# Kernel tuning notes

Hardware: AMD Instinct MI355X
Metric: run time of the kernel (lower is better)

The kernel has to match this reference:

```python
import jax, jax.numpy as jnp
import numpy as np

D_MODEL = 1024
N_HEAD = 16
ATT_DIM = D_MODEL // N_HEAD


def setup_inputs() -> dict:
    key = jax.random.key(0)
    ks = jax.random.split(key, 7)
    B, S = 2, 2048
    q = jax.random.normal(ks[0], (B, S, D_MODEL), dtype=jnp.float32)
    k = jax.random.normal(ks[1], (B, S, D_MODEL), dtype=jnp.float32)
    v = jax.random.normal(ks[2], (B, S, D_MODEL), dtype=jnp.float32)
    # per-head projection weights, stored as [H, d_model, att_dim] (x @ W form)
    scale_qkv = float(np.sqrt(6.0 / (D_MODEL + ATT_DIM)))  # xavier_uniform
    Wq = jax.random.uniform(ks[3], (N_HEAD, D_MODEL, ATT_DIM), jnp.float32, -scale_qkv, scale_qkv)
    Wk = jax.random.uniform(ks[4], (N_HEAD, D_MODEL, ATT_DIM), jnp.float32, -scale_qkv, scale_qkv)
    Wv = jax.random.uniform(ks[5], (N_HEAD, D_MODEL, ATT_DIM), jnp.float32, -scale_qkv, scale_qkv)
    scale_o = float(np.sqrt(6.0 / (D_MODEL + D_MODEL)))
    Wo = jax.random.uniform(ks[6], (D_MODEL, D_MODEL), jnp.float32, -scale_o, scale_o)
    return {"q": q, "k": k, "v": v, "Wq": Wq, "Wk": Wk, "Wv": Wv, "Wo": Wo}


def reference(q, k, v, Wq, Wk, Wv, Wo):
    # per-head projections, batched over heads: [H,B,S,E]
    qh = jnp.einsum('bsd,hde->hbse', q, Wq)
    kh = jnp.einsum('bsd,hde->hbse', k, Wk)
    vh = jnp.einsum('bsd,hde->hbse', v, Wv)
    # NOTE: original divides by att_dim (not sqrt(att_dim))
    scores = jnp.einsum('hbqe,hbke->hbqk', qh, kh) / ATT_DIM
    attn = jax.nn.softmax(scores, axis=-1)  # [H,B,Sq,Sk]
    att = jnp.einsum('hbqk,hbke->hbqe', attn, vh)  # [H,B,S,E]
    # concat heads along last dim in head order, then output projection
    H, B, S, E = att.shape
    cat = jnp.transpose(att, (1, 2, 0, 3)).reshape(B, S, H * E)
    out = cat @ Wo  # dropout is identity in eval
    return (out, attn)
```

## Files before the change

kernel.cpp:

```cpp
#include <hip/hip_runtime.h>
#include <hip/hip_bf16.h>

#define DM 1024
#define NH 16
#define AD 64
#define BB 2
#define SS 2048
#define LOG2E 1.44269504f

typedef float f32x4 __attribute__((ext_vector_type(4)));
typedef short bf16x8 __attribute__((ext_vector_type(8)));
typedef unsigned short u16;
typedef unsigned int u32;
typedef u16 u16x4 __attribute__((ext_vector_type(4)));
typedef u16 u16x8 __attribute__((ext_vector_type(8)));
typedef u32 u32x4 __attribute__((ext_vector_type(4)));

static __device__ __forceinline__ u16 f2bf(float f) {
  unsigned u = __builtin_bit_cast(unsigned, f);
  u += 0x7fffu + ((u >> 16) & 1u);
  return (u16)(u >> 16);
}

#define MFMA16(a, b, c) __builtin_amdgcn_mfma_f32_16x16x32_bf16((a), (b), (c), 0, 0, 0)

static __device__ __forceinline__ void ld_lds16(const void* g, void* l) {
  __builtin_amdgcn_global_load_lds((const __attribute__((address_space(1))) u32*)g,
                                   (__attribute__((address_space(3))) u32*)l, 16, 0, 0);
}

#define WAITV(N)                                             \
  do {                                                       \
    asm volatile("s_waitcnt vmcnt(" #N ")" ::: "memory");    \
    __builtin_amdgcn_sched_barrier(0);                       \
  } while (0)
#define WAITL0()                                             \
  do {                                                       \
    asm volatile("s_waitcnt lgkmcnt(0)" ::: "memory");       \
    __builtin_amdgcn_sched_barrier(0);                       \
  } while (0)
#define BAR() __builtin_amdgcn_s_barrier()

#define KFRAG(buf, row, P) (*(const bf16x8*)(&(buf)[(row) * 64 + ((((P) ^ ((row) & 7))) << 3)]))
#define V64(buf, row, P, hh) \
  (*(const u16x4*)(&(buf)[(row) * 64 + ((((P) ^ ((row) & 7))) << 3) + (hh) * 4]))

__global__ __launch_bounds__(256, 4) void cast3_kernel(const float* __restrict__ s0,
                                                       const float* __restrict__ s1,
                                                       const float* __restrict__ s2,
                                                       u16* __restrict__ d0, u16* __restrict__ d1,
                                                       u16* __restrict__ d2, int n8) {
  const float* src = blockIdx.y == 0 ? s0 : blockIdx.y == 1 ? s1 : s2;
  u16* dst = blockIdx.y == 0 ? d0 : blockIdx.y == 1 ? d1 : d2;
  int i = blockIdx.x * blockDim.x + threadIdx.x;
  int stride = gridDim.x * blockDim.x;
  for (; i < n8; i += stride) {
    const f32x4* p = (const f32x4*)src + 2 * (size_t)i;
    f32x4 a = p[0], b = p[1];
    u16x8 o;
    o[0] = f2bf(a[0]); o[1] = f2bf(a[1]); o[2] = f2bf(a[2]); o[3] = f2bf(a[3]);
    o[4] = f2bf(b[0]); o[5] = f2bf(b[1]); o[6] = f2bf(b[2]); o[7] = f2bf(b[3]);
    *((u16x8*)dst + i) = o;
  }
}

template <int MODE>
__global__ __launch_bounds__(256, 4) void tcast_kernel(const float* __restrict__ s0,
                                                       const float* __restrict__ s1,
                                                       const float* __restrict__ s2,
                                                       u16* __restrict__ dst, int R, int C,
                                                       float scale0) {
  __shared__ float T[64][65];
  const float* src;
  u16* dstp;
  float scale;
  long bo;
  if (MODE == 0) {
    src = s0; bo = (long)blockIdx.z * R * C; dstp = dst; scale = scale0;
  } else {
    int which = blockIdx.z >> 4, zz = blockIdx.z & 15;
    src = which == 0 ? s0 : which == 1 ? s1 : s2;
    bo = (long)zz * R * C;
    dstp = dst + (long)which * NH * R * C;
    scale = which == 0 ? scale0 : 1.0f;
  }
  int r0 = blockIdx.x * 64, c0 = blockIdx.y * 64;
  int cl = threadIdx.x & 63, rl = threadIdx.x >> 6;
#pragma unroll
  for (int i = 0; i < 16; i++) {
    int rr = rl + 4 * i;
    T[cl][rr] = src[bo + (long)(r0 + rr) * C + c0 + cl];
  }
  __syncthreads();
#pragma unroll
  for (int i = 0; i < 16; i++) {
    int cc = rl + 4 * i;
    dstp[bo + (long)(c0 + cc) * R + r0 + cl] = f2bf(T[cc][cl] * scale);
  }
}

__global__ __launch_bounds__(256, 3) void qkvproj_kernel(const u16* __restrict__ X0,
                                                         const u16* __restrict__ WT0,
                                                         u16* __restrict__ out0) {
  __shared__ u16 Ab[2][128 * 64];
  __shared__ u16 Bb[2][64 * 64];
  const long NX = (long)BB * SS * DM;
  const long NW = (long)NH * DM * AD;
  int which = blockIdx.z;
  int sg0 = blockIdx.x * 128;
  int b = sg0 >> 11, s0 = sg0 & (SS - 1);
  int h = blockIdx.y;
  int tid = threadIdx.x, w = tid >> 6, lane = tid & 63, g = lane >> 4, li = lane & 15;
  const u16* xb = X0 + (long)which * NX + ((long)b * SS + s0) * DM;
  const u16* wb = WT0 + (long)which * NW + (long)h * 64 * DM;
  u16* outp = out0 + (long)which * NX;

  const u16* asrc[4];
  u16* adst[2][4];
#pragma unroll
  for (int i = 0; i < 4; i++) {
    int cc = i * 256 + tid;
    int row = cc >> 3, sp = (cc ^ (row & 7)) & 7;
    asrc[i] = xb + (long)row * DM + sp * 8;
    adst[0][i] = &Ab[0][cc * 8];
    adst[1][i] = &Ab[1][cc * 8];
  }
  const u16* bsrc[2];
  u16* bdst[2][2];
#pragma unroll
  for (int i = 0; i < 2; i++) {
    int cc = i * 256 + tid;
    int row = cc >> 3, sp = (cc ^ (row & 7)) & 7;
    bsrc[i] = wb + (long)row * DM + sp * 8;
    bdst[0][i] = &Bb[0][cc * 8];
    bdst[1][i] = &Bb[1][cc * 8];
  }

#pragma unroll
  for (int i = 0; i < 4; i++) ld_lds16(asrc[i], adst[0][i]);
#pragma unroll
  for (int i = 0; i < 2; i++) ld_lds16(bsrc[i], bdst[0][i]);

  f32x4 acc[2][4] = {};
  for (int kc = 0; kc < DM / 64; kc++) {
    int cur = kc & 1;
    if (kc + 1 < DM / 64) {
      int ko = (kc + 1) * 64;
#pragma unroll
      for (int i = 0; i < 4; i++) ld_lds16(asrc[i] + ko, adst[cur ^ 1][i]);
#pragma unroll
      for (int i = 0; i < 2; i++) ld_lds16(bsrc[i] + ko, bdst[cur ^ 1][i]);
      WAITV(6);
    } else {
      WAITV(0);
    }
    BAR();
    const u16* ab = Ab[cur];
    const u16* bb = Bb[cur];
#pragma unroll
    for (int kk = 0; kk < 2; kk++) {
      bf16x8 bf[4];
#pragma unroll
      for (int j = 0; j < 4; j++) bf[j] = KFRAG(bb, j * 16 + li, kk * 4 + g);
#pragma unroll
      for (int mi = 0; mi < 2; mi++) {
        bf16x8 af = KFRAG(ab, w * 32 + mi * 16 + li, kk * 4 + g);
#pragma unroll
        for (int j = 0; j < 4; j++) acc[mi][j] = MFMA16(af, bf[j], acc[mi][j]);
      }
    }
    WAITL0();
    BAR();
  }

  long obase = (long)h * (BB * SS * AD) + (long)b * (SS * AD);
#pragma unroll
  for (int mi = 0; mi < 2; mi++) {
    int sb = s0 + w * 32 + mi * 16 + 4 * g;
#pragma unroll
    for (int j = 0; j < 4; j++) {
      int e = j * 16 + li;
      if (which < 2) {
#pragma unroll
        for (int r = 0; r < 4; r++)
          outp[obase + (long)(sb + r) * AD + e] = f2bf(acc[mi][j][r]);
      } else {
        u16x4 vv;
#pragma unroll
        for (int r = 0; r < 4; r++) vv[r] = f2bf(acc[mi][j][r]);
        *(u16x4*)(outp + obase + (long)e * SS + sb) = vv;
      }
    }
  }
}

__global__ __launch_bounds__(256, 3) void outproj_kernel(const u16* __restrict__ X,
                                                         const u16* __restrict__ WT,
                                                         float* __restrict__ out) {
  __shared__ u16 Ab[2][128 * 64];
  __shared__ u16 Bb[2][64 * 64];
  int sg0 = blockIdx.x * 128;
  int n0 = blockIdx.y * 64;
  int tid = threadIdx.x, w = tid >> 6, lane = tid & 63, g = lane >> 4, li = lane & 15;
  const u16* xb = X + (long)sg0 * DM;
  const u16* wb = WT + (long)n0 * DM;

  const u16* asrc[4];
  u16* adst[2][4];
#pragma unroll
  for (int i = 0; i < 4; i++) {
    int cc = i * 256 + tid;
    int row = cc >> 3, sp = (cc ^ (row & 7)) & 7;
    asrc[i] = xb + (long)row * DM + sp * 8;
    adst[0][i] = &Ab[0][cc * 8];
    adst[1][i] = &Ab[1][cc * 8];
  }
  const u16* bsrc[2];
  u16* bdst[2][2];
#pragma unroll
  for (int i = 0; i < 2; i++) {
    int cc = i * 256 + tid;
    int row = cc >> 3, sp = (cc ^ (row & 7)) & 7;
    bsrc[i] = wb + (long)row * DM + sp * 8;
    bdst[0][i] = &Bb[0][cc * 8];
    bdst[1][i] = &Bb[1][cc * 8];
  }

#pragma unroll
  for (int i = 0; i < 4; i++) ld_lds16(asrc[i], adst[0][i]);
#pragma unroll
  for (int i = 0; i < 2; i++) ld_lds16(bsrc[i], bdst[0][i]);

  f32x4 acc[2][4] = {};
  for (int kc = 0; kc < DM / 64; kc++) {
    int cur = kc & 1;
    if (kc + 1 < DM / 64) {
      int ko = (kc + 1) * 64;
#pragma unroll
      for (int i = 0; i < 4; i++) ld_lds16(asrc[i] + ko, adst[cur ^ 1][i]);
#pragma unroll
      for (int i = 0; i < 2; i++) ld_lds16(bsrc[i] + ko, bdst[cur ^ 1][i]);
      WAITV(6);
    } else {
      WAITV(0);
    }
    BAR();
    const u16* ab = Ab[cur];
    const u16* bb = Bb[cur];
#pragma unroll
    for (int kk = 0; kk < 2; kk++) {
      bf16x8 bf[4];
#pragma unroll
      for (int j = 0; j < 4; j++) bf[j] = KFRAG(bb, j * 16 + li, kk * 4 + g);
#pragma unroll
      for (int mi = 0; mi < 2; mi++) {
        bf16x8 af = KFRAG(ab, w * 32 + mi * 16 + li, kk * 4 + g);
#pragma unroll
        for (int j = 0; j < 4; j++) acc[mi][j] = MFMA16(af, bf[j], acc[mi][j]);
      }
    }
    WAITL0();
    BAR();
  }

#pragma unroll
  for (int mi = 0; mi < 2; mi++) {
    int sb = sg0 + w * 32 + mi * 16 + 4 * g;
#pragma unroll
    for (int j = 0; j < 4; j++) {
      int col = n0 + j * 16 + li;
#pragma unroll
      for (int r = 0; r < 4; r++) out[(long)(sb + r) * DM + col] = acc[mi][j][r];
    }
  }
}

__global__ __launch_bounds__(512, 4) void attn_kernel(const u16* __restrict__ qh,
                                                      const u16* __restrict__ kh,
                                                      const u16* __restrict__ vhT,
                                                      float* __restrict__ attn_out,
                                                      u16* __restrict__ cat) {
  __shared__ u16 Kb[2][64 * 64];
  __shared__ u16 Vb[2][64 * 64];
  int h = blockIdx.y, b = blockIdx.z;
  int hb = h * BB + b;
  int tid = threadIdx.x;
  int w = tid >> 6, lane = tid & 63;
  int g = lane >> 4, li = lane & 15;
  long base = (long)hb * SS * AD;
  const u16* qhb = qh + base;
  const u16* khb = kh + base;
  const u16* vhb = vhT + base;
  int q0 = blockIdx.x * 128 + w * 16;

  bf16x8 bq0 = *(const bf16x8*)(qhb + (q0 + li) * AD + 8 * g);
  bf16x8 bq1 = *(const bf16x8*)(qhb + (q0 + li) * AD + 32 + 8 * g);

  int srow = tid >> 3, spiece = (tid ^ (srow & 7)) & 7;
  const u16* ksrc = khb + (long)srow * AD + spiece * 8;
  const u16* vsrc = vhb + (long)srow * SS + spiece * 8;
  u16* kd0 = &Kb[0][tid * 8]; u16* kd1 = &Kb[1][tid * 8];
  u16* vd0 = &Vb[0][tid * 8]; u16* vd1 = &Vb[1][tid * 8];

  float l_run = 0.f;
  ld_lds16(ksrc, kd0);
  ld_lds16(ksrc + 64 * AD, kd1);
  ld_lds16(ksrc + 2 * 64 * AD, vd0);
  for (int ch4 = 0; ch4 < SS / 64; ch4 += 4) {
#pragma unroll
    for (int u = 0; u < 4; u++) {
      int ch = ch4 + u;
      u16* pdst = ((u + 3) & 3) == 0 ? kd0 : ((u + 3) & 3) == 1 ? kd1
                 : ((u + 3) & 3) == 2 ? vd0 : vd1;
      if (ch + 3 < SS / 64) {
        ld_lds16(ksrc + (ch + 3) * 64 * AD, pdst);
        WAITV(3);
      } else if (ch == SS / 64 - 3) {
        WAITV(2);
      } else if (ch == SS / 64 - 2) {
        WAITV(1);
      } else {
        WAITV(0);
      }
      BAR();
      const u16* kb = u == 0 ? Kb[0] : u == 1 ? Kb[1] : u == 2 ? Vb[0] : Vb[1];
      f32x4 sacc[4] = {};
#pragma unroll
      for (int mi = 0; mi < 4; mi++) {
        bf16x8 a0 = KFRAG(kb, mi * 16 + li, g);
        bf16x8 a1 = KFRAG(kb, mi * 16 + li, 4 + g);
        sacc[mi] = MFMA16(a0, bq0, sacc[mi]);
        sacc[mi] = MFMA16(a1, bq1, sacc[mi]);
      }
#pragma unroll
      for (int c = 0; c < 4; c++)
#pragma unroll
        for (int r = 0; r < 4; r++) l_run += exp2f(sacc[c][r]);
      WAITL0();
      BAR();
    }
  }
  l_run += __shfl_xor(l_run, 16);
  l_run += __shfl_xor(l_run, 32);
  float moff = log2f(l_run);

  ld_lds16(ksrc, kd0);
  ld_lds16(vsrc, vd0);
  f32x4 accv[4] = {};
  float* arow = attn_out + ((long)hb * SS + q0 + li) * SS;
  for (int ch2 = 0; ch2 < SS / 64; ch2 += 2) {
#pragma unroll
    for (int u = 0; u < 2; u++) {
      int ch = ch2 + u;
      u16* kpd = u ? kd0 : kd1;
      u16* vpd = u ? vd0 : vd1;
      if (ch + 1 < SS / 64) {
        ld_lds16(ksrc + (ch + 1) * 64 * AD, kpd);
        ld_lds16(vsrc + (ch + 1) * 64, vpd);
        if (ch == 0) {
          WAITV(2);
        } else {
          WAITV(6);
        }
      } else {
        WAITV(4);
      }
      BAR();
      const u16* kb = Kb[u];
      const u16* vb = Vb[u];
      f32x4 sacc[4] = {};
#pragma unroll
      for (int mi = 0; mi < 4; mi++) {
        bf16x8 a0 = KFRAG(kb, mi * 16 + li, g);
        bf16x8 a1 = KFRAG(kb, mi * 16 + li, 4 + g);
        sacc[mi] = MFMA16(a0, bq0, sacc[mi]);
        sacc[mi] = MFMA16(a1, bq1, sacc[mi]);
      }
      u32 pw[8];
#pragma unroll
      for (int c = 0; c < 4; c++) {
        f32x4 pv;
#pragma unroll
        for (int r = 0; r < 4; r++) pv[r] = exp2f(sacc[c][r] - moff);
        *(f32x4*)(arow + ch * 64 + c * 16 + 4 * g) = pv;
        pw[2 * c] = (u32)f2bf(pv[0]) | ((u32)f2bf(pv[1]) << 16);
        pw[2 * c + 1] = (u32)f2bf(pv[2]) | ((u32)f2bf(pv[3]) << 16);
      }
#pragma unroll
      for (int kk = 0; kk < 2; kk++) {
        u32x4 aw = {pw[4 * kk], pw[4 * kk + 1], pw[4 * kk + 2], pw[4 * kk + 3]};
        bf16x8 ap = __builtin_bit_cast(bf16x8, aw);
#pragma unroll
        for (int et = 0; et < 4; et++) {
          int row = et * 16 + li;
          u16x4 b0 = V64(vb, row, 4 * kk + (g >> 1), g & 1);
          u16x4 b1 = V64(vb, row, 4 * kk + 2 + (g >> 1), g & 1);
          u16x8 ub = {b0[0], b0[1], b0[2], b0[3], b1[0], b1[1], b1[2], b1[3]};
          bf16x8 bv = __builtin_bit_cast(bf16x8, ub);
          accv[et] = MFMA16(ap, bv, accv[et]);
        }
      }
      WAITL0();
      BAR();
    }
  }

#pragma unroll
  for (int et = 0; et < 4; et++)
#pragma unroll
    for (int r = 0; r < 4; r++)
      cat[((long)b * SS + q0 + 4 * g + r) * DM + h * AD + et * 16 + li] = f2bf(accv[et][r]);
}

extern "C" void kernel_launch(void* const* d_in, const int* in_sizes, int n_in, void* d_out,
                              int out_size, void* d_ws, size_t ws_size, hipStream_t stream) {
  const float* q = (const float*)d_in[0];
  const float* k = (const float*)d_in[1];
  const float* v = (const float*)d_in[2];
  const float* Wq = (const float*)d_in[3];
  const float* Wk = (const float*)d_in[4];
  const float* Wv = (const float*)d_in[5];
  const float* Wo = (const float*)d_in[6];
  float* out = (float*)d_out;
  float* attn_out = out + (long)BB * SS * DM;

  const long NX = (long)BB * SS * DM;
  const long NW = (long)NH * DM * AD;
  u16* ws = (u16*)d_ws;
  u16* xq = ws;
  u16* xk = xq + NX;
  u16* xv = xk + NX;
  u16* WqT = xv + NX;
  u16* WkT = WqT + NW;
  u16* WvT = WkT + NW;
  u16* WoT = WvT + NW;
  u16* qhw = WoT + (long)DM * DM;
  u16* khw = qhw + NX;
  u16* vhw = khw + NX;
  u16* catw = vhw + NX;

  (void)xk; (void)xv; (void)WkT; (void)WvT; (void)khw;

  cast3_kernel<<<dim3(700, 3), 256, 0, stream>>>(q, k, v, xq, xk, xv, (int)(NX / 8));
  tcast_kernel<1><<<dim3(16, 1, 48), 256, 0, stream>>>(Wq, Wk, Wv, WqT, DM, AD, LOG2E / AD);
  tcast_kernel<0><<<dim3(16, 16, 1), 256, 0, stream>>>(Wo, nullptr, nullptr, WoT, DM, DM, 1.0f);

  qkvproj_kernel<<<dim3(BB * SS / 128, NH, 3), 256, 0, stream>>>(xq, WqT, qhw);

  attn_kernel<<<dim3(SS / 128, NH, BB), 512, 0, stream>>>(qhw, khw, vhw, attn_out, catw);

  outproj_kernel<<<dim3(BB * SS / 128, DM / 64), 256, 0, stream>>>(catw, WoT, out);
}
```

Measured before the change: 283.6 us.

## Halve attention block size, add MFMA priority hints and nontemporal attn stores

Attention blocks shrink from 512 to 256 threads, each covering 64 query rows instead of 128. Every thread now issues two async K/V tile loads per stage, so the wait counts are retuned to match. s_setprio raises wave priority around the MFMA sections in the attention and projection GEMM loops, and the large fp32 attention-probability writes become nontemporal stores to avoid polluting the cache. The smaller blocks give more blocks and finer scheduling, at the cost of each K/V tile being loaded from global memory twice as often overall.

```diff
diff --git a/kernel.cpp b/kernel.cpp
--- a/kernel.cpp
+++ b/kernel.cpp
@@ -157,6 +157,7 @@
     BAR();
     const u16* ab = Ab[cur];
     const u16* bb = Bb[cur];
+    __builtin_amdgcn_s_setprio(1);
 #pragma unroll
     for (int kk = 0; kk < 2; kk++) {
       bf16x8 bf[4];
@@ -169,6 +170,7 @@
         for (int j = 0; j < 4; j++) acc[mi][j] = MFMA16(af, bf[j], acc[mi][j]);
       }
     }
+    __builtin_amdgcn_s_setprio(0);
     WAITL0();
     BAR();
   }
@@ -247,6 +249,7 @@
     BAR();
     const u16* ab = Ab[cur];
     const u16* bb = Bb[cur];
+    __builtin_amdgcn_s_setprio(1);
 #pragma unroll
     for (int kk = 0; kk < 2; kk++) {
       bf16x8 bf[4];
@@ -259,6 +262,7 @@
         for (int j = 0; j < 4; j++) acc[mi][j] = MFMA16(af, bf[j], acc[mi][j]);
       }
     }
+    __builtin_amdgcn_s_setprio(0);
     WAITL0();
     BAR();
   }
@@ -275,7 +279,7 @@
   }
 }
 
-__global__ __launch_bounds__(512, 4) void attn_kernel(const u16* __restrict__ qh,
+__global__ __launch_bounds__(256, 4) void attn_kernel(const u16* __restrict__ qh,
                                                       const u16* __restrict__ kh,
                                                       const u16* __restrict__ vhT,
                                                       float* __restrict__ attn_out,
@@ -291,40 +295,48 @@
   const u16* qhb = qh + base;
   const u16* khb = kh + base;
   const u16* vhb = vhT + base;
-  int q0 = blockIdx.x * 128 + w * 16;
+  int q0 = blockIdx.x * 64 + w * 16;
 
   bf16x8 bq0 = *(const bf16x8*)(qhb + (q0 + li) * AD + 8 * g);
   bf16x8 bq1 = *(const bf16x8*)(qhb + (q0 + li) * AD + 32 + 8 * g);
 
-  int srow = tid >> 3, spiece = (tid ^ (srow & 7)) & 7;
-  const u16* ksrc = khb + (long)srow * AD + spiece * 8;
-  const u16* vsrc = vhb + (long)srow * SS + spiece * 8;
-  u16* kd0 = &Kb[0][tid * 8]; u16* kd1 = &Kb[1][tid * 8];
-  u16* vd0 = &Vb[0][tid * 8]; u16* vd1 = &Vb[1][tid * 8];
+  int r1 = tid >> 3, p1 = (tid ^ (r1 & 7)) & 7;
+  int r2 = (tid + 256) >> 3, p2 = ((tid + 256) ^ (r2 & 7)) & 7;
+  const u16* ks1 = khb + (long)r1 * AD + p1 * 8;
+  const u16* ks2 = khb + (long)r2 * AD + p2 * 8;
+  const u16* vs1 = vhb + (long)r1 * SS + p1 * 8;
+  const u16* vs2 = vhb + (long)r2 * SS + p2 * 8;
+  u16* kd0a = &Kb[0][tid * 8]; u16* kd0b = &Kb[0][(tid + 256) * 8];
+  u16* kd1a = &Kb[1][tid * 8]; u16* kd1b = &Kb[1][(tid + 256) * 8];
+  u16* vd0a = &Vb[0][tid * 8]; u16* vd0b = &Vb[0][(tid + 256) * 8];
+  u16* vd1a = &Vb[1][tid * 8]; u16* vd1b = &Vb[1][(tid + 256) * 8];
 
   float l_run = 0.f;
-  ld_lds16(ksrc, kd0);
-  ld_lds16(ksrc + 64 * AD, kd1);
-  ld_lds16(ksrc + 2 * 64 * AD, vd0);
+  ld_lds16(ks1, kd0a); ld_lds16(ks2, kd0b);
+  ld_lds16(ks1 + 64 * AD, kd1a); ld_lds16(ks2 + 64 * AD, kd1b);
+  ld_lds16(ks1 + 2 * 64 * AD, vd0a); ld_lds16(ks2 + 2 * 64 * AD, vd0b);
   for (int ch4 = 0; ch4 < SS / 64; ch4 += 4) {
 #pragma unroll
     for (int u = 0; u < 4; u++) {
       int ch = ch4 + u;
-      u16* pdst = ((u + 3) & 3) == 0 ? kd0 : ((u + 3) & 3) == 1 ? kd1
-                 : ((u + 3) & 3) == 2 ? vd0 : vd1;
+      int slot = (u + 3) & 3;
+      u16* pa = slot == 0 ? kd0a : slot == 1 ? kd1a : slot == 2 ? vd0a : vd1a;
+      u16* pb = slot == 0 ? kd0b : slot == 1 ? kd1b : slot == 2 ? vd0b : vd1b;
       if (ch + 3 < SS / 64) {
-        ld_lds16(ksrc + (ch + 3) * 64 * AD, pdst);
-        WAITV(3);
+        ld_lds16(ks1 + (ch + 3) * 64 * AD, pa);
+        ld_lds16(ks2 + (ch + 3) * 64 * AD, pb);
+        WAITV(6);
       } else if (ch == SS / 64 - 3) {
+        WAITV(4);
+      } else if (ch == SS / 64 - 2) {
         WAITV(2);
-      } else if (ch == SS / 64 - 2) {
-        WAITV(1);
       } else {
         WAITV(0);
       }
       BAR();
       const u16* kb = u == 0 ? Kb[0] : u == 1 ? Kb[1] : u == 2 ? Vb[0] : Vb[1];
       f32x4 sacc[4] = {};
+      __builtin_amdgcn_s_setprio(1);
 #pragma unroll
       for (int mi = 0; mi < 4; mi++) {
         bf16x8 a0 = KFRAG(kb, mi * 16 + li, g);
@@ -332,6 +344,7 @@
         sacc[mi] = MFMA16(a0, bq0, sacc[mi]);
         sacc[mi] = MFMA16(a1, bq1, sacc[mi]);
       }
+      __builtin_amdgcn_s_setprio(0);
 #pragma unroll
       for (int c = 0; c < 4; c++)
 #pragma unroll
@@ -344,23 +357,25 @@
   l_run += __shfl_xor(l_run, 32);
   float moff = log2f(l_run);
 
-  ld_lds16(ksrc, kd0);
-  ld_lds16(vsrc, vd0);
+  ld_lds16(ks1, kd0a); ld_lds16(ks2, kd0b);
+  ld_lds16(vs1, vd0a); ld_lds16(vs2, vd0b);
   f32x4 accv[4] = {};
   float* arow = attn_out + ((long)hb * SS + q0 + li) * SS;
   for (int ch2 = 0; ch2 < SS / 64; ch2 += 2) {
 #pragma unroll
     for (int u = 0; u < 2; u++) {
       int ch = ch2 + u;
-      u16* kpd = u ? kd0 : kd1;
-      u16* vpd = u ? vd0 : vd1;
+      u16* kpa = u ? kd0a : kd1a; u16* kpb = u ? kd0b : kd1b;
+      u16* vpa = u ? vd0a : vd1a; u16* vpb = u ? vd0b : vd1b;
       if (ch + 1 < SS / 64) {
-        ld_lds16(ksrc + (ch + 1) * 64 * AD, kpd);
-        ld_lds16(vsrc + (ch + 1) * 64, vpd);
+        ld_lds16(ks1 + (ch + 1) * 64 * AD, kpa);
+        ld_lds16(ks2 + (ch + 1) * 64 * AD, kpb);
+        ld_lds16(vs1 + (ch + 1) * 64, vpa);
+        ld_lds16(vs2 + (ch + 1) * 64, vpb);
         if (ch == 0) {
-          WAITV(2);
+          WAITV(4);
         } else {
-          WAITV(6);
+          WAITV(8);
         }
       } else {
         WAITV(4);
@@ -369,6 +384,7 @@
       const u16* kb = Kb[u];
       const u16* vb = Vb[u];
       f32x4 sacc[4] = {};
+      __builtin_amdgcn_s_setprio(1);
 #pragma unroll
       for (int mi = 0; mi < 4; mi++) {
         bf16x8 a0 = KFRAG(kb, mi * 16 + li, g);
@@ -376,13 +392,14 @@
         sacc[mi] = MFMA16(a0, bq0, sacc[mi]);
         sacc[mi] = MFMA16(a1, bq1, sacc[mi]);
       }
+      __builtin_amdgcn_s_setprio(0);
       u32 pw[8];
 #pragma unroll
       for (int c = 0; c < 4; c++) {
         f32x4 pv;
 #pragma unroll
         for (int r = 0; r < 4; r++) pv[r] = exp2f(sacc[c][r] - moff);
-        *(f32x4*)(arow + ch * 64 + c * 16 + 4 * g) = pv;
+        __builtin_nontemporal_store(pv, (f32x4*)(arow + ch * 64 + c * 16 + 4 * g));
         pw[2 * c] = (u32)f2bf(pv[0]) | ((u32)f2bf(pv[1]) << 16);
         pw[2 * c + 1] = (u32)f2bf(pv[2]) | ((u32)f2bf(pv[3]) << 16);
       }
@@ -439,7 +456,7 @@
   u16* vhw = khw + NX;
   u16* catw = vhw + NX;
 
-  (void)xk; (void)xv; (void)WkT; (void)WvT; (void)khw;
+  (void)xk; (void)xv; (void)WkT; (void)WvT;
 
   cast3_kernel<<<dim3(700, 3), 256, 0, stream>>>(q, k, v, xq, xk, xv, (int)(NX / 8));
   tcast_kernel<1><<<dim3(16, 1, 48), 256, 0, stream>>>(Wq, Wk, Wv, WqT, DM, AD, LOG2E / AD);
@@ -447,7 +464,7 @@
 
   qkvproj_kernel<<<dim3(BB * SS / 128, NH, 3), 256, 0, stream>>>(xq, WqT, qhw);
 
-  attn_kernel<<<dim3(SS / 128, NH, BB), 512, 0, stream>>>(qhw, khw, vhw, attn_out, catw);
+  attn_kernel<<<dim3(SS / 64, NH, BB), 256, 0, stream>>>(qhw, khw, vhw, attn_out, catw);
 
   outproj_kernel<<<dim3(BB * SS / 128, DM / 64), 256, 0, stream>>>(catw, WoT, out);
 }
```

Result: faster. 259.1 us, median of 2 (-8.6%).
